# Kernel tuning notes

Measured on AMD Instinct MI355X. Metric: run time of the kernel, lower is better.

Reference implementation:

```python
import jax, jax.numpy as jnp
import numpy as np

NEG_SLOPE = 0.2  # PyG GATConv default leaky_relu slope


def gat_conv(h_in, src, dst, W, a_src, a_dst, b, N):
    # h_in: [N, Fin]; src/dst: [E] (self-loops already appended)
    h = h_in @ W                      # [N, Fout]
    alpha_src = h @ a_src             # [N]
    alpha_dst = h @ a_dst             # [N]
    e = jax.nn.leaky_relu(alpha_src[src] + alpha_dst[dst], NEG_SLOPE)  # [E]
    # segment softmax over incoming edges of each destination node
    m = jax.ops.segment_max(e, dst, num_segments=N)
    m = jnp.where(jnp.isfinite(m), m, 0.0)
    p = jnp.exp(e - m[dst])
    denom = jax.ops.segment_sum(p, dst, num_segments=N)
    alpha = p / jnp.maximum(denom[dst], 1e-16)
    out = jax.ops.segment_sum(alpha[:, None] * h[src], dst, num_segments=N)
    return out + b


def setup_inputs() -> dict:
    key = jax.random.key(0)
    ks = jax.random.split(key, 16)
    N, E, V, D, H, C, G = 100000, 1600000, 128, 50, 16, 10, 512
    x = jax.random.normal(ks[0], (N, V), dtype=jnp.float32)
    edge_index = jax.random.randint(ks[1], (2, E), 0, N, dtype=jnp.int32)
    batch = jnp.sort(jax.random.randint(ks[2], (N,), 0, G, dtype=jnp.int32))
    s = lambda fan: 1.0 / np.sqrt(fan)
    return {
        "x": x, "edge_index": edge_index, "batch": batch,
        "embedding": jax.random.normal(ks[3], (V, D), dtype=jnp.float32),
        "W1": jax.random.normal(ks[4], (D, H), dtype=jnp.float32) * s(D),
        "a_src1": jax.random.normal(ks[5], (H,), dtype=jnp.float32) * s(H),
        "a_dst1": jax.random.normal(ks[6], (H,), dtype=jnp.float32) * s(H),
        "b1": jnp.zeros((H,), dtype=jnp.float32),
        "W2": jax.random.normal(ks[7], (H, H), dtype=jnp.float32) * s(H),
        "a_src2": jax.random.normal(ks[8], (H,), dtype=jnp.float32) * s(H),
        "a_dst2": jax.random.normal(ks[9], (H,), dtype=jnp.float32) * s(H),
        "b2": jnp.zeros((H,), dtype=jnp.float32),
        "W3": jax.random.normal(ks[10], (H, C), dtype=jnp.float32) * s(H),
        "a_src3": jax.random.normal(ks[11], (C,), dtype=jnp.float32) * s(C),
        "a_dst3": jax.random.normal(ks[12], (C,), dtype=jnp.float32) * s(C),
        "b3": jnp.zeros((C,), dtype=jnp.float32),
    }


def reference(x, edge_index, batch, embedding, W1, a_src1, a_dst1, b1,
              W2, a_src2, a_dst2, b2, W3, a_src3, a_dst3, b3):
    N = x.shape[0]
    G = 512  # num graphs
    # embedding lookup via argmax over one-hot-ish features
    idx = jnp.argmax(x, axis=1)
    h = embedding[idx]                               # [N, 50]
    # add self-loops once (PyG GATConv default)
    loops = jnp.arange(N, dtype=edge_index.dtype)
    src = jnp.concatenate([edge_index[0], loops])
    dst = jnp.concatenate([edge_index[1], loops])
    h = jax.nn.relu(gat_conv(h, src, dst, W1, a_src1, a_dst1, b1, N))
    # dropout: eval mode -> identity
    h = jax.nn.relu(gat_conv(h, src, dst, W2, a_src2, a_dst2, b2, N))
    h = gat_conv(h, src, dst, W3, a_src3, a_dst3, b3, N)  # [N, C]
    # global mean pool over graphs
    sums = jax.ops.segment_sum(h, batch, num_segments=G)
    cnts = jax.ops.segment_sum(jnp.ones((N,), h.dtype), batch, num_segments=G)
    pooled = sums / jnp.maximum(cnts, 1.0)[:, None]
    return jax.nn.softmax(pooled, axis=1)
```

## Files before the change

### kernel.cpp

```cpp
#include <hip/hip_runtime.h>
#include <math.h>

#define NEG_SLOPE 0.2f
#define NBUK_MAX 512

typedef float v4f __attribute__((ext_vector_type(4)));
typedef _Float16 h4v __attribute__((ext_vector_type(4)));


template <int B2>
__global__ void __launch_bounds__(1024)
k_histarg(const float* __restrict__ x, const int* __restrict__ edst, int E,
          int* __restrict__ histT, int NBUK, int* __restrict__ idx, int N, int V) {
    __shared__ int sh[NBUK_MAX];
    int t = threadIdx.x;
    if ((int)blockIdx.x < B2) {
        int b = blockIdx.x;
        for (int k = t; k < NBUK; k += 1024) sh[k] = 0;
        __syncthreads();
        long long ebeg = (long long)b * E / B2, eend = (long long)(b + 1) * E / B2;
        for (long long i = ebeg + t; i < eend; i += 1024)
            atomicAdd(&sh[__builtin_nontemporal_load(&edst[i]) >> 8], 1);
        __syncthreads();
        for (int k = t; k < NBUK; k += 1024) histT[(long long)k * B2 + b] = sh[k];
    } else {
        int node = ((int)blockIdx.x - B2) * 32 + (t >> 5);
        int lane = t & 31;
        if (node >= N) return;
        const v4f* row = (const v4f*)(x + (long long)node * V);
        float bv = -INFINITY;
        int bi = 0x7fffffff;
        int nq = V >> 2;
        for (int q = lane; q < nq; q += 32) {
            v4f v = __builtin_nontemporal_load(&row[q]);
            int base = q << 2;
            if (v.x > bv || (v.x == bv && base     < bi)) { bv = v.x; bi = base;     }
            if (v.y > bv || (v.y == bv && base + 1 < bi)) { bv = v.y; bi = base + 1; }
            if (v.z > bv || (v.z == bv && base + 2 < bi)) { bv = v.z; bi = base + 2; }
            if (v.w > bv || (v.w == bv && base + 3 < bi)) { bv = v.w; bi = base + 3; }
        }
        for (int off = 16; off > 0; off >>= 1) {
            float ov = __shfl_down(bv, off, 32);
            int   oi = __shfl_down(bi, off, 32);
            if (ov > bv || (ov == bv && oi < bi)) { bv = ov; bi = oi; }
        }
        if (lane == 0) idx[node] = bi;
    }
}

template <int FIN, int FOUT>
__global__ void __launch_bounds__(256)
k_scan_tr(const int* __restrict__ vals, int* __restrict__ excl, int* __restrict__ bsums, int M,
          const float* __restrict__ emb, const int* __restrict__ idx,
          const float* __restrict__ W, const float* __restrict__ a_src,
          const float* __restrict__ a_dst, _Float16* __restrict__ hT,
          float* __restrict__ asrc, int4* __restrict__ meta,
          int N, int NB_SCAN) {
    __shared__ int s[256];
    __shared__ float sW[FIN * FOUT];
    __shared__ float sa[FOUT], sd[FOUT];
    int t = threadIdx.x;
    if ((int)blockIdx.x < NB_SCAN) {
        int i = blockIdx.x * 256 + t;
        int v = (i < M) ? vals[i] : 0;
        s[t] = v;
        __syncthreads();
        for (int off = 1; off < 256; off <<= 1) {
            int a = (t >= off) ? s[t - off] : 0;
            __syncthreads();
            s[t] += a;
            __syncthreads();
        }
        if (i < M) excl[i] = s[t] - v;
        if (t == 255) bsums[blockIdx.x] = s[255];
    } else {
        for (int i = t; i < FIN * FOUT; i += 256) sW[i] = W[i];
        if (t < FOUT) { sa[t] = a_src[t]; sd[t] = a_dst[t]; }
        __syncthreads();
        int n = ((int)blockIdx.x - NB_SCAN) * 256 + t;
        if (n >= N) return;
        float acc[FOUT];
#pragma unroll
        for (int f = 0; f < FOUT; f++) acc[f] = 0.f;
        const float* hr = emb + (long long)idx[n] * FIN;
        for (int k = 0; k < FIN; k++) {
            float v = hr[k];
#pragma unroll
            for (int f = 0; f < FOUT; f++) acc[f] += v * sW[k * FOUT + f];
        }
        float s1 = 0.f, s2 = 0.f;
        _Float16 hh[16];
#pragma unroll
        for (int f = 0; f < 16; f++) hh[f] = (_Float16)0.f;
#pragma unroll
        for (int f = 0; f < FOUT; f++) {
            hh[f] = (_Float16)acc[f];
            s1 += acc[f] * sa[f];
            s2 += acc[f] * sd[f];
        }
        uint4* hrow = (uint4*)(hT + (long long)n * 16);
        hrow[0] = ((uint4*)hh)[0];
        hrow[1] = ((uint4*)hh)[1];
        asrc[n] = s1;
        float2 am; am.x = s1; am.y = s2;
        *(float2*)&meta[n] = am;
    }
}

template <int B2>
__global__ void __launch_bounds__(1024)
k_scatB(const int* __restrict__ esrc, const int* __restrict__ edst, int E,
        const int* __restrict__ sexcl, const int* __restrict__ bsums,
        int* __restrict__ tmp, int NBUK) {
    __shared__ int cur[NBUK_MAX];
    __shared__ int bex[512];
    int t = threadIdx.x, b = blockIdx.x;
    if (t < 512) bex[t] = (t < NBUK) ? bsums[t] : 0;
    __syncthreads();
    for (int off = 1; off < 512; off <<= 1) {
        int a = (t < 512 && t >= off) ? bex[t - off] : 0;
        __syncthreads();
        if (t < 512) bex[t] += a;
        __syncthreads();
    }
    for (int k = t; k < NBUK; k += 1024)
        cur[k] = sexcl[(long long)k * B2 + b] + (k ? bex[k - 1] : 0);
    __syncthreads();
    long long ebeg = (long long)b * E / B2, eend = (long long)(b + 1) * E / B2;
    for (long long i = ebeg + t; i < eend; i += 1024) {
        int d = __builtin_nontemporal_load(&edst[i]);
        int sv = __builtin_nontemporal_load(&esrc[i]);
        int pos = atomicAdd(&cur[d >> 8], 1);
        tmp[pos] = ((d & 255) << 17) | sv;
    }
}

template <int B2>
__global__ void __launch_bounds__(512)
k_binB(const int* __restrict__ sexcl, const int* __restrict__ bsums,
       const int* __restrict__ tmp, int* __restrict__ perm, int4* __restrict__ meta,
       int* __restrict__ csr_src, int N, int NBUK, int E) {
    __shared__ int bx[512];
    __shared__ int cnt[256];
    __shared__ int h1[256];
    __shared__ int h2[256];
    __shared__ int sdv[256];
    __shared__ int ssc[256];
    __shared__ int cur[256];
    int t = threadIdx.x, b = blockIdx.x;
    bx[t] = (t < NBUK) ? bsums[t] : 0;
    __syncthreads();
    for (int off = 1; off < 512; off <<= 1) {
        int a = (t >= off) ? bx[t - off] : 0;
        __syncthreads();
        bx[t] += a;
        __syncthreads();
    }
    int t0 = sexcl[(long long)b * B2] + (b ? bx[b - 1] : 0);
    int t1 = (b + 1 < NBUK) ? (sexcl[(long long)(b + 1) * B2] + bx[b]) : E;
    if (t < 256) cnt[t] = 0;
    __syncthreads();
    for (int i = t0 + t; i < t1; i += 512)
        atomicAdd(&cnt[__builtin_nontemporal_load(&tmp[i]) >> 17], 1);
    __syncthreads();
    int d = b * 256 + t;
    bool valid = (t < 256) && (d < N);
    int dg = (t < 256) ? cnt[t] : 0;

    if (t < 256) h1[t] = 0;
    __syncthreads();
    int key = 255 - min(dg, 255);
    if (valid) atomicAdd(&h1[key], 1);
    __syncthreads();
    int v = (t < 256) ? h1[t] : 0;
    if (t < 256) h2[t] = v;
    __syncthreads();
    for (int off = 1; off < 256; off <<= 1) {
        int a = (t < 256 && t >= off) ? h2[t - off] : 0;
        __syncthreads();
        if (t < 256) h2[t] += a;
        __syncthreads();
    }
    if (t < 256) h1[t] = h2[t] - v;
    __syncthreads();
    int r = 0;
    if (valid) r = atomicAdd(&h1[key], 1);

    if (t < 256) sdv[t] = 0;
    __syncthreads();
    if (valid) sdv[r] = dg;
    __syncthreads();
    int sv = (t < 256) ? sdv[t] : 0;
    if (t < 256) ssc[t] = sv;
    __syncthreads();
    for (int off = 1; off < 256; off <<= 1) {
        int a = (t < 256 && t >= off) ? ssc[t - off] : 0;
        __syncthreads();
        if (t < 256) ssc[t] += a;
        __syncthreads();
    }
    if (valid) {
        int base = t0 + ssc[r] - dg;
        cur[t] = base;
        perm[b * 256 + r] = d;
        int2 m; m.x = base; m.y = base + dg;
        *(int2*)((char*)&meta[d] + 8) = m;
    }
    __syncthreads();
    for (int i = t0 + t; i < t1; i += 512) {
        int p = __builtin_nontemporal_load(&tmp[i]);
        int pos = atomicAdd(&cur[p >> 17], 1);
        csr_src[pos] = p & 0x1FFFF;
    }
}

template <typename EPI>
__device__ __forceinline__ void gat_core4(const _Float16* __restrict__ hT,
                                          const float* __restrict__ asrc,
                                          const int4* __restrict__ meta,
                                          const int* __restrict__ csr_src,
                                          int d, int l4, EPI epilogue) {
    const char* __restrict__ Hb = (const char*)hT;
    int4 m = meta[d];
    float as_d = __int_as_float(m.x);
    float ad   = __int_as_float(m.y);
    int r0 = m.z, r1 = m.w;

    float e0 = as_d + ad;
    e0 = (e0 >= 0.f) ? e0 : NEG_SLOPE * e0;
    float p0 = __expf(e0);
    h4v hd = *(const h4v*)(Hb + (((unsigned)d) << 5) + (l4 << 3));
    float a0 = p0 * (float)hd[0], a1 = p0 * (float)hd[1];
    float a2 = p0 * (float)hd[2], a3 = p0 * (float)hd[3];
    float psum = (l4 == 0) ? p0 : 0.f;

    int rem = r1 - r0;
    if (rem > 0) {
        int nch = (rem + 3) >> 2;

#define GLOAD(S, AV, c) do { \
        int jj = r0 + ((c) << 2) + l4; \
        int jc = (jj < r1) ? jj : r0; \
        int sr = __builtin_nontemporal_load(&csr_src[jc]); \
        S = (jj < r1) ? sr : d; \
        AV = asrc[S]; } while (0)

#define GMID(S, AV, P0, P1, P2, P3, H0, H1, H2, H3, c) do { \
        int jj = r0 + ((c) << 2) + l4; \
        float e = AV + ad; e = (e >= 0.f) ? e : NEG_SLOPE * e; \
        float p = (jj < r1) ? __expf(e) : 0.f; \
        psum += p; \
        P0 = __shfl(p, 0, 4); { int sk = __shfl(S, 0, 4); H0 = *(const h4v*)(Hb + (((unsigned)sk) << 5) + (l4 << 3)); } \
        P1 = __shfl(p, 1, 4); { int sk = __shfl(S, 1, 4); H1 = *(const h4v*)(Hb + (((unsigned)sk) << 5) + (l4 << 3)); } \
        P2 = __shfl(p, 2, 4); { int sk = __shfl(S, 2, 4); H2 = *(const h4v*)(Hb + (((unsigned)sk) << 5) + (l4 << 3)); } \
        P3 = __shfl(p, 3, 4); { int sk = __shfl(S, 3, 4); H3 = *(const h4v*)(Hb + (((unsigned)sk) << 5) + (l4 << 3)); } } while (0)

#define GFMA(P0, P1, P2, P3, H0, H1, H2, H3) do { \
        a0 += P0 * (float)H0[0]; a1 += P0 * (float)H0[1]; a2 += P0 * (float)H0[2]; a3 += P0 * (float)H0[3]; \
        a0 += P1 * (float)H1[0]; a1 += P1 * (float)H1[1]; a2 += P1 * (float)H1[2]; a3 += P1 * (float)H1[3]; \
        a0 += P2 * (float)H2[0]; a1 += P2 * (float)H2[1]; a2 += P2 * (float)H2[2]; a3 += P2 * (float)H2[3]; \
        a0 += P3 * (float)H3[0]; a1 += P3 * (float)H3[1]; a2 += P3 * (float)H3[2]; a3 += P3 * (float)H3[3]; } while (0)

        int   sA, sB, sC = d;
        float avA, avB, avC = 0.f;
        float pA0, pA1, pA2, pA3, pB0, pB1, pB2, pB3;
        h4v   hA0, hA1, hA2, hA3, hB0, hB1, hB2, hB3;

        GLOAD(sA, avA, 0);
        if (nch > 1) GLOAD(sB, avB, 1);
        GMID(sA, avA, pA0, pA1, pA2, pA3, hA0, hA1, hA2, hA3, 0);
        int c = 0;
        while (c + 1 < nch) {
            if (c + 2 < nch) GLOAD(sC, avC, c + 2);
            GMID(sB, avB, pB0, pB1, pB2, pB3, hB0, hB1, hB2, hB3, c + 1);
            GFMA(pA0, pA1, pA2, pA3, hA0, hA1, hA2, hA3);
            pA0 = pB0; pA1 = pB1; pA2 = pB2; pA3 = pB3;
            hA0 = hB0; hA1 = hB1; hA2 = hB2; hA3 = hB3;
            sB = sC; avB = avC;
            c++;
        }
        GFMA(pA0, pA1, pA2, pA3, hA0, hA1, hA2, hA3);
#undef GLOAD
#undef GMID
#undef GFMA
    }
    psum += __shfl_xor(psum, 1, 4);
    psum += __shfl_xor(psum, 2, 4);
    float inv = 1.f / fmaxf(psum, 1e-16f);
    epilogue(d, r0, r1, a0 * inv, a1 * inv, a2 * inv, a3 * inv);
}

template <int FN>
__global__ void __launch_bounds__(256)
k_gat_ft(const _Float16* __restrict__ hT, const float* __restrict__ asrc,
         const int4* __restrict__ meta, const int* __restrict__ csr_src,
         const int* __restrict__ perm, const float* __restrict__ bias,
         const float* __restrict__ Wn, const float* __restrict__ an_src,
         const float* __restrict__ an_dst,
         _Float16* __restrict__ hT_n, float* __restrict__ asrc_n,
         int4* __restrict__ meta_n, int N) {
    __shared__ float sW[16 * 16];
    __shared__ float sa[16], sd[16], sb[16];
    int t = threadIdx.x;
    {
        int k = t >> 4, f = t & 15;
        sW[t] = (f < FN) ? Wn[k * FN + f] : 0.f;
    }
    if (t < 16) {
        sa[t] = (t < FN) ? an_src[t] : 0.f;
        sd[t] = (t < FN) ? an_dst[t] : 0.f;
        sb[t] = bias[t];
    }
    __syncthreads();

    int gid = blockIdx.x * 256 + t;
    int grp = gid >> 2, l4 = gid & 3;
    if (grp >= N) return;
    int d = perm[grp];

    gat_core4(hT, asrc, meta, csr_src, d, l4,
        [&](int dd, int r0, int r1, float v0, float v1, float v2, float v3) {
            int f0 = l4 * 4;
            float vv[4];
            vv[0] = fmaxf(v0 + sb[f0    ], 0.f);
            vv[1] = fmaxf(v1 + sb[f0 + 1], 0.f);
            vv[2] = fmaxf(v2 + sb[f0 + 2], 0.f);
            vv[3] = fmaxf(v3 + sb[f0 + 3], 0.f);
            float o0 = 0.f, o1 = 0.f, o2 = 0.f, o3 = 0.f;
#pragma unroll
            for (int q = 0; q < 4; q++) {
#pragma unroll
                for (int i = 0; i < 4; i++) {
                    float vk = __shfl(vv[i], q, 4);
                    const float* wr = &sW[(q * 4 + i) * 16 + f0];
                    o0 += vk * wr[0];
                    o1 += vk * wr[1];
                    o2 += vk * wr[2];
                    o3 += vk * wr[3];
                }
            }
            float c1 = o0 * sa[f0] + o1 * sa[f0 + 1] + o2 * sa[f0 + 2] + o3 * sa[f0 + 3];
            float c2 = o0 * sd[f0] + o1 * sd[f0 + 1] + o2 * sd[f0 + 2] + o3 * sd[f0 + 3];
            c1 += __shfl_xor(c1, 1, 4); c1 += __shfl_xor(c1, 2, 4);
            c2 += __shfl_xor(c2, 1, 4); c2 += __shfl_xor(c2, 2, 4);
            h4v ho = { (_Float16)o0, (_Float16)o1, (_Float16)o2, (_Float16)o3 };
            ((h4v*)hT_n)[(long long)dd * 4 + l4] = ho;
            if (l4 == 0) {
                asrc_n[dd] = c1;
                int4 mm;
                mm.x = __float_as_int(c1); mm.y = __float_as_int(c2);
                mm.z = r0; mm.w = r1;
                meta_n[dd] = mm;
            }
        });
}

__global__ void __launch_bounds__(256)
k_gat_last(const _Float16* __restrict__ hT, const float* __restrict__ asrc,
           const int4* __restrict__ meta, const int* __restrict__ csr_src,
           const int* __restrict__ perm, float* __restrict__ out, int N) {
    int gid = blockIdx.x * 256 + threadIdx.x;
    int grp = gid >> 2, l4 = gid & 3;
    if (grp >= N) return;
    int d = perm[grp];
    gat_core4(hT, asrc, meta, csr_src, d, l4,
        [&](int dd, int r0, int r1, float v0, float v1, float v2, float v3) {
            v4f o = { v0, v1, v2, v3 };
            ((v4f*)out)[(long long)dd * 4 + l4] = o;
        });
}

__global__ void k_pool(const float* __restrict__ h3, const int* __restrict__ batch,
                       const float* __restrict__ b3, float* __restrict__ out, int N, int C) {
    int g = blockIdx.x;
    int lo = 0, hi = N;
    while (lo < hi) { int mid = (lo + hi) >> 1; if (batch[mid] < g) lo = mid + 1; else hi = mid; }
    int start = lo;
    hi = N;
    while (lo < hi) { int mid = (lo + hi) >> 1; if (batch[mid] < g + 1) lo = mid + 1; else hi = mid; }
    int end = lo;

    float sum[16];
    for (int f = 0; f < C; f++) sum[f] = 0.f;
    for (int n = start + threadIdx.x; n < end; n += blockDim.x) {
        const float* r = h3 + (long long)n * 16;
        for (int f = 0; f < C; f++) sum[f] += r[f];
    }
    __shared__ float red[256 * 16];
    for (int f = 0; f < C; f++) red[threadIdx.x * 16 + f] = sum[f];
    __syncthreads();
    for (int str = blockDim.x / 2; str > 0; str >>= 1) {
        if ((int)threadIdx.x < str)
            for (int f = 0; f < C; f++) red[threadIdx.x * 16 + f] += red[(threadIdx.x + str) * 16 + f];
        __syncthreads();
    }
    if (threadIdx.x == 0) {
        float cnt = fmaxf((float)(end - start), 1.f);
        float vals[16];
        float mx = -INFINITY;
        for (int f = 0; f < C; f++) { vals[f] = red[f] / cnt + b3[f]; mx = fmaxf(mx, vals[f]); }
        float se = 0.f;
        for (int f = 0; f < C; f++) { vals[f] = __expf(vals[f] - mx); se += vals[f]; }
        for (int f = 0; f < C; f++) out[(long long)g * C + f] = vals[f] / se;
    }
}

extern "C" void kernel_launch(void* const* d_in, const int* in_sizes, int n_in,
                              void* d_out, int out_size, void* d_ws, size_t ws_size,
                              hipStream_t stream) {
    const float* x    = (const float*)d_in[0];
    const int*   eidx = (const int*)d_in[1];
    const int*   batch= (const int*)d_in[2];
    const float* emb  = (const float*)d_in[3];
    const float* W1   = (const float*)d_in[4];
    const float* as1  = (const float*)d_in[5];
    const float* ad1  = (const float*)d_in[6];
    const float* b1   = (const float*)d_in[7];
    const float* W2   = (const float*)d_in[8];
    const float* as2  = (const float*)d_in[9];
    const float* ad2  = (const float*)d_in[10];
    const float* b2   = (const float*)d_in[11];
    const float* W3   = (const float*)d_in[12];
    const float* as3  = (const float*)d_in[13];
    const float* ad3  = (const float*)d_in[14];
    const float* b3   = (const float*)d_in[15];

    const int H = in_sizes[5];
    const int C = in_sizes[13];
    const int D = in_sizes[4] / H;
    const int V = in_sizes[3] / D;
    const int N = in_sizes[0] / V;
    const int E = in_sizes[1] / 2;
    const int G = out_size / C;
    const int* esrc = eidx;
    const int* edst = eidx + E;
    const int NBUK = (N + 255) >> 8;
    constexpr int B2 = 256;
    const int M = NBUK * B2;

    char* w = (char*)d_ws;
    auto carve = [&](size_t bytes) {
        char* p = w;
        w += (bytes + 255) & ~(size_t)255;
        return p;
    };
    int*      idx     = (int*)carve((size_t)N * 4);
    int*      perm    = (int*)carve((size_t)N * 4);
    int*      histT   = (int*)carve((size_t)M * 4);
    int*      sexcl   = (int*)carve((size_t)M * 4);
    int*      bsums   = (int*)carve(2048 * 4);
    int*      csr_src = (int*)carve((size_t)E * 4);
    _Float16* hTa     = (_Float16*)carve((size_t)N * 32);
    _Float16* hTb     = (_Float16*)carve((size_t)N * 32);
    float*    asA     = (float*)carve((size_t)N * 4);
    float*    asB     = (float*)carve((size_t)N * 4);
    int4*     metaA   = (int4*)carve((size_t)N * 16);
    int4*     metaB   = (int4*)carve((size_t)N * 16);
    size_t zone_bytes = ((size_t)E * 4 > (size_t)N * 64) ? (size_t)E * 4 : (size_t)N * 64;
    char*  zone = carve(zone_bytes);
    float* X0  = (float*)zone;
    int*   tmp = (int*)zone;
    (void)ws_size; (void)n_in;

    const int BT = 256;
    dim3 blk(BT);
    int gGat4 = (N * 4 + BT - 1) / BT;
    int nb2   = (M + 255) / 256;
    int gArg  = (N + 31) / 32;
    int gTr   = (N + BT - 1) / BT;

    k_histarg<B2><<<B2 + gArg, dim3(1024), 0, stream>>>(x, edst, E, histT, NBUK, idx, N, V);

    k_scan_tr<50, 16><<<nb2 + gTr, blk, 0, stream>>>(histT, sexcl, bsums, M,
                                                     emb, idx, W1, as1, ad1,
                                                     hTa, asA, metaA, N, nb2);

    k_scatB<B2><<<B2, dim3(1024), 0, stream>>>(esrc, edst, E, sexcl, bsums, tmp, NBUK);
    k_binB<B2><<<NBUK, dim3(512), 0, stream>>>(sexcl, bsums, tmp, perm, metaA, csr_src, N, NBUK, E);

    k_gat_ft<16><<<gGat4, blk, 0, stream>>>(hTa, asA, metaA, csr_src, perm, b1,
                                            W2, as2, ad2, hTb, asB, metaB, N);

    k_gat_ft<10><<<gGat4, blk, 0, stream>>>(hTb, asB, metaB, csr_src, perm, b2,
                                            W3, as3, ad3, hTa, asA, metaA, N);

    k_gat_last<<<gGat4, blk, 0, stream>>>(hTa, asA, metaA, csr_src, perm, X0, N);

    k_pool<<<G, blk, 0, stream>>>(X0, batch, b3, (float*)d_out, N, C);
}
```

Measured before the change: 311.5 us.

## Recompute source attention logits from gathered fp16 features instead of gathering asrc

Removes the per-node asrc arrays and, for each edge, rebuilds the source attention score as a dot product of the gathered fp16 feature row with a_src, reduced across the 4-lane group by shuffles. This drops one dependent random gather per edge (asrc[src]) and the writes that filled asrc, so each edge needs only the csr index load and then the feature load. In exchange it adds per-edge shuffles and FMAs, serializes exp on each feature fetch, and computes the logit from fp16-rounded features, which slightly changes numerics.

```diff
diff --git a/kernel.cpp b/kernel.cpp
--- a/kernel.cpp
+++ b/kernel.cpp
@@ -54,8 +54,7 @@
           const float* __restrict__ emb, const int* __restrict__ idx,
           const float* __restrict__ W, const float* __restrict__ a_src,
           const float* __restrict__ a_dst, _Float16* __restrict__ hT,
-          float* __restrict__ asrc, int4* __restrict__ meta,
-          int N, int NB_SCAN) {
+          int4* __restrict__ meta, int N, int NB_SCAN) {
     __shared__ int s[256];
     __shared__ float sW[FIN * FOUT];
     __shared__ float sa[FOUT], sd[FOUT];
@@ -101,7 +100,6 @@
         uint4* hrow = (uint4*)(hT + (long long)n * 16);
         hrow[0] = ((uint4*)hh)[0];
         hrow[1] = ((uint4*)hh)[1];
-        asrc[n] = s1;
         float2 am; am.x = s1; am.y = s2;
         *(float2*)&meta[n] = am;
     }
@@ -216,7 +214,7 @@
 
 template <typename EPI>
 __device__ __forceinline__ void gat_core4(const _Float16* __restrict__ hT,
-                                          const float* __restrict__ asrc,
+                                          v4f aw,
                                           const int4* __restrict__ meta,
                                           const int* __restrict__ csr_src,
                                           int d, int l4, EPI epilogue) {
@@ -232,73 +230,72 @@
     h4v hd = *(const h4v*)(Hb + (((unsigned)d) << 5) + (l4 << 3));
     float a0 = p0 * (float)hd[0], a1 = p0 * (float)hd[1];
     float a2 = p0 * (float)hd[2], a3 = p0 * (float)hd[3];
-    float psum = (l4 == 0) ? p0 : 0.f;
+    float psum = p0;
 
     int rem = r1 - r0;
     if (rem > 0) {
         int nch = (rem + 3) >> 2;
 
-#define GLOAD(S, AV, c) do { \
+#define SLOAD(S, c) do { \
         int jj = r0 + ((c) << 2) + l4; \
         int jc = (jj < r1) ? jj : r0; \
         int sr = __builtin_nontemporal_load(&csr_src[jc]); \
-        S = (jj < r1) ? sr : d; \
-        AV = asrc[S]; } while (0)
-
-#define GMID(S, AV, P0, P1, P2, P3, H0, H1, H2, H3, c) do { \
-        int jj = r0 + ((c) << 2) + l4; \
-        float e = AV + ad; e = (e >= 0.f) ? e : NEG_SLOPE * e; \
-        float p = (jj < r1) ? __expf(e) : 0.f; \
+        S = (jj < r1) ? sr : d; } while (0)
+
+#define HGATH(S, H0, H1, H2, H3) do { \
+        { int sk = __shfl(S, 0, 4); H0 = *(const h4v*)(Hb + (((unsigned)sk) << 5) + (l4 << 3)); } \
+        { int sk = __shfl(S, 1, 4); H1 = *(const h4v*)(Hb + (((unsigned)sk) << 5) + (l4 << 3)); } \
+        { int sk = __shfl(S, 2, 4); H2 = *(const h4v*)(Hb + (((unsigned)sk) << 5) + (l4 << 3)); } \
+        { int sk = __shfl(S, 3, 4); H3 = *(const h4v*)(Hb + (((unsigned)sk) << 5) + (l4 << 3)); } } while (0)
+
+#define PEDGE(Hk, kk, c) do { \
+        float f0 = (float)Hk[0], f1 = (float)Hk[1], f2 = (float)Hk[2], f3 = (float)Hk[3]; \
+        float dt = f0 * aw.x + f1 * aw.y + f2 * aw.z + f3 * aw.w; \
+        dt += __shfl_xor(dt, 1, 4); \
+        dt += __shfl_xor(dt, 2, 4); \
+        float e = dt + ad; \
+        e = (e >= 0.f) ? e : NEG_SLOPE * e; \
+        float p = (r0 + ((c) << 2) + (kk) < r1) ? __expf(e) : 0.f; \
         psum += p; \
-        P0 = __shfl(p, 0, 4); { int sk = __shfl(S, 0, 4); H0 = *(const h4v*)(Hb + (((unsigned)sk) << 5) + (l4 << 3)); } \
-        P1 = __shfl(p, 1, 4); { int sk = __shfl(S, 1, 4); H1 = *(const h4v*)(Hb + (((unsigned)sk) << 5) + (l4 << 3)); } \
-        P2 = __shfl(p, 2, 4); { int sk = __shfl(S, 2, 4); H2 = *(const h4v*)(Hb + (((unsigned)sk) << 5) + (l4 << 3)); } \
-        P3 = __shfl(p, 3, 4); { int sk = __shfl(S, 3, 4); H3 = *(const h4v*)(Hb + (((unsigned)sk) << 5) + (l4 << 3)); } } while (0)
-
-#define GFMA(P0, P1, P2, P3, H0, H1, H2, H3) do { \
-        a0 += P0 * (float)H0[0]; a1 += P0 * (float)H0[1]; a2 += P0 * (float)H0[2]; a3 += P0 * (float)H0[3]; \
-        a0 += P1 * (float)H1[0]; a1 += P1 * (float)H1[1]; a2 += P1 * (float)H1[2]; a3 += P1 * (float)H1[3]; \
-        a0 += P2 * (float)H2[0]; a1 += P2 * (float)H2[1]; a2 += P2 * (float)H2[2]; a3 += P2 * (float)H2[3]; \
-        a0 += P3 * (float)H3[0]; a1 += P3 * (float)H3[1]; a2 += P3 * (float)H3[2]; a3 += P3 * (float)H3[3]; } while (0)
-
-        int   sA, sB, sC = d;
-        float avA, avB, avC = 0.f;
-        float pA0, pA1, pA2, pA3, pB0, pB1, pB2, pB3;
-        h4v   hA0, hA1, hA2, hA3, hB0, hB1, hB2, hB3;
-
-        GLOAD(sA, avA, 0);
-        if (nch > 1) GLOAD(sB, avB, 1);
-        GMID(sA, avA, pA0, pA1, pA2, pA3, hA0, hA1, hA2, hA3, 0);
+        a0 += p * f0; a1 += p * f1; a2 += p * f2; a3 += p * f3; } while (0)
+
+#define PROC(H0, H1, H2, H3, c) do { \
+        PEDGE(H0, 0, c); PEDGE(H1, 1, c); PEDGE(H2, 2, c); PEDGE(H3, 3, c); } while (0)
+
+        int sA, sB = d, sC = d;
+        h4v hA0, hA1, hA2, hA3, hB0, hB1, hB2, hB3;
+
+        SLOAD(sA, 0);
+        HGATH(sA, hA0, hA1, hA2, hA3);
+        if (nch > 1) SLOAD(sB, 1);
         int c = 0;
         while (c + 1 < nch) {
-            if (c + 2 < nch) GLOAD(sC, avC, c + 2);
-            GMID(sB, avB, pB0, pB1, pB2, pB3, hB0, hB1, hB2, hB3, c + 1);
-            GFMA(pA0, pA1, pA2, pA3, hA0, hA1, hA2, hA3);
-            pA0 = pB0; pA1 = pB1; pA2 = pB2; pA3 = pB3;
+            if (c + 2 < nch) SLOAD(sC, c + 2);
+            HGATH(sB, hB0, hB1, hB2, hB3);
+            PROC(hA0, hA1, hA2, hA3, c);
             hA0 = hB0; hA1 = hB1; hA2 = hB2; hA3 = hB3;
-            sB = sC; avB = avC;
+            sB = sC;
             c++;
         }
-        GFMA(pA0, pA1, pA2, pA3, hA0, hA1, hA2, hA3);
-#undef GLOAD
-#undef GMID
-#undef GFMA
-    }
-    psum += __shfl_xor(psum, 1, 4);
-    psum += __shfl_xor(psum, 2, 4);
+        PROC(hA0, hA1, hA2, hA3, c);
+#undef SLOAD
+#undef HGATH
+#undef PEDGE
+#undef PROC
+    }
     float inv = 1.f / fmaxf(psum, 1e-16f);
     epilogue(d, r0, r1, a0 * inv, a1 * inv, a2 * inv, a3 * inv);
 }
 
 template <int FN>
 __global__ void __launch_bounds__(256)
-k_gat_ft(const _Float16* __restrict__ hT, const float* __restrict__ asrc,
-         const int4* __restrict__ meta, const int* __restrict__ csr_src,
-         const int* __restrict__ perm, const float* __restrict__ bias,
+k_gat_ft(const _Float16* __restrict__ hT, const int4* __restrict__ meta,
+         const int* __restrict__ csr_src, const int* __restrict__ perm,
+         const float* __restrict__ a_cur,
+         const float* __restrict__ bias,
          const float* __restrict__ Wn, const float* __restrict__ an_src,
          const float* __restrict__ an_dst,
-         _Float16* __restrict__ hT_n, float* __restrict__ asrc_n,
-         int4* __restrict__ meta_n, int N) {
+         _Float16* __restrict__ hT_n, int4* __restrict__ meta_n, int N) {
     __shared__ float sW[16 * 16];
     __shared__ float sa[16], sd[16], sb[16];
     int t = threadIdx.x;
@@ -317,8 +314,10 @@
     int grp = gid >> 2, l4 = gid & 3;
     if (grp >= N) return;
     int d = perm[grp];
-
-    gat_core4(hT, asrc, meta, csr_src, d, l4,
+    int fb = l4 << 2;
+    v4f aw = { a_cur[fb], a_cur[fb + 1], a_cur[fb + 2], a_cur[fb + 3] };
+
+    gat_core4(hT, aw, meta, csr_src, d, l4,
         [&](int dd, int r0, int r1, float v0, float v1, float v2, float v3) {
             int f0 = l4 * 4;
             float vv[4];
@@ -346,7 +345,6 @@
             h4v ho = { (_Float16)o0, (_Float16)o1, (_Float16)o2, (_Float16)o3 };
             ((h4v*)hT_n)[(long long)dd * 4 + l4] = ho;
             if (l4 == 0) {
-                asrc_n[dd] = c1;
                 int4 mm;
                 mm.x = __float_as_int(c1); mm.y = __float_as_int(c2);
                 mm.z = r0; mm.w = r1;
@@ -355,15 +353,22 @@
         });
 }
 
+template <int FC>
 __global__ void __launch_bounds__(256)
-k_gat_last(const _Float16* __restrict__ hT, const float* __restrict__ asrc,
-           const int4* __restrict__ meta, const int* __restrict__ csr_src,
-           const int* __restrict__ perm, float* __restrict__ out, int N) {
+k_gat_last(const _Float16* __restrict__ hT, const int4* __restrict__ meta,
+           const int* __restrict__ csr_src, const int* __restrict__ perm,
+           const float* __restrict__ a_cur, float* __restrict__ out, int N) {
     int gid = blockIdx.x * 256 + threadIdx.x;
     int grp = gid >> 2, l4 = gid & 3;
     if (grp >= N) return;
     int d = perm[grp];
-    gat_core4(hT, asrc, meta, csr_src, d, l4,
+    int fb = l4 << 2;
+    v4f aw;
+    aw.x = (fb     < FC) ? a_cur[fb]     : 0.f;
+    aw.y = (fb + 1 < FC) ? a_cur[fb + 1] : 0.f;
+    aw.z = (fb + 2 < FC) ? a_cur[fb + 2] : 0.f;
+    aw.w = (fb + 3 < FC) ? a_cur[fb + 3] : 0.f;
+    gat_core4(hT, aw, meta, csr_src, d, l4,
         [&](int dd, int r0, int r1, float v0, float v1, float v2, float v3) {
             v4f o = { v0, v1, v2, v3 };
             ((v4f*)out)[(long long)dd * 4 + l4] = o;
@@ -452,8 +457,6 @@
     int*      csr_src = (int*)carve((size_t)E * 4);
     _Float16* hTa     = (_Float16*)carve((size_t)N * 32);
     _Float16* hTb     = (_Float16*)carve((size_t)N * 32);
-    float*    asA     = (float*)carve((size_t)N * 4);
-    float*    asB     = (float*)carve((size_t)N * 4);
     int4*     metaA   = (int4*)carve((size_t)N * 16);
     int4*     metaB   = (int4*)carve((size_t)N * 16);
     size_t zone_bytes = ((size_t)E * 4 > (size_t)N * 64) ? (size_t)E * 4 : (size_t)N * 64;
@@ -473,18 +476,18 @@
 
     k_scan_tr<50, 16><<<nb2 + gTr, blk, 0, stream>>>(histT, sexcl, bsums, M,
                                                      emb, idx, W1, as1, ad1,
-                                                     hTa, asA, metaA, N, nb2);
+                                                     hTa, metaA, N, nb2);
 
     k_scatB<B2><<<B2, dim3(1024), 0, stream>>>(esrc, edst, E, sexcl, bsums, tmp, NBUK);
     k_binB<B2><<<NBUK, dim3(512), 0, stream>>>(sexcl, bsums, tmp, perm, metaA, csr_src, N, NBUK, E);
 
-    k_gat_ft<16><<<gGat4, blk, 0, stream>>>(hTa, asA, metaA, csr_src, perm, b1,
-                                            W2, as2, ad2, hTb, asB, metaB, N);
-
-    k_gat_ft<10><<<gGat4, blk, 0, stream>>>(hTb, asB, metaB, csr_src, perm, b2,
-                                            W3, as3, ad3, hTa, asA, metaA, N);
-
-    k_gat_last<<<gGat4, blk, 0, stream>>>(hTa, asA, metaA, csr_src, perm, X0, N);
+    k_gat_ft<16><<<gGat4, blk, 0, stream>>>(hTa, metaA, csr_src, perm, as1, b1,
+                                            W2, as2, ad2, hTb, metaB, N);
+
+    k_gat_ft<10><<<gGat4, blk, 0, stream>>>(hTb, metaB, csr_src, perm, as2, b2,
+                                            W3, as3, ad3, hTa, metaA, N);
+
+    k_gat_last<10><<<gGat4, blk, 0, stream>>>(hTa, metaA, csr_src, perm, as3, X0, N);
 
     k_pool<<<G, blk, 0, stream>>>(X0, batch, b3, (float*)d_out, N, C);
 }
```

Measured after the change: 278.8 us. 1.12x faster.
